# Performance work log

Hardware: AMD Instinct MI355X
Metric: run time of the kernel (lower is better)

## Reference

```python
import jax, jax.numpy as jnp
import numpy as np

N_NODES = 50000
N_EDGES = 1600000
IN_FEATS = 512
N_HIDDEN = 128
N_CLASSES = 40


def setup_inputs() -> dict:
    key = jax.random.key(0)
    k1, k2, k3, k4, k5, k6, k7 = jax.random.split(key, 7)
    features = jax.random.normal(k1, (N_NODES, IN_FEATS), dtype=jnp.float32)
    src = jax.random.randint(k2, (N_EDGES,), 0, N_NODES)
    dst = jax.random.randint(k3, (N_EDGES,), 0, N_NODES)
    # Glorot-ish init for weights, zeros for biases (DGL GraphConv defaults)
    W1 = jax.random.normal(k4, (IN_FEATS, N_HIDDEN), dtype=jnp.float32) / np.sqrt(IN_FEATS)
    b1 = jnp.zeros((N_HIDDEN,), dtype=jnp.float32)
    W2 = jax.random.normal(k5, (N_HIDDEN, N_CLASSES), dtype=jnp.float32) / np.sqrt(N_HIDDEN)
    b2 = jnp.zeros((N_CLASSES,), dtype=jnp.float32)
    return {"features": features, "W1": W1, "b1": b1, "W2": W2, "b2": b2,
            "src": src, "dst": dst}


def _norms(src, dst, n_nodes):
    ones = jnp.ones(src.shape[0], dtype=jnp.float32)
    deg_out = jax.ops.segment_sum(ones, src, num_segments=n_nodes)
    deg_in = jax.ops.segment_sum(ones, dst, num_segments=n_nodes)
    # clamp degree >= 1 as DGL does
    norm_src = jax.lax.rsqrt(jnp.maximum(deg_out, 1.0))
    norm_dst = jax.lax.rsqrt(jnp.maximum(deg_in, 1.0))
    return norm_src, norm_dst


def _graph_conv(x, W, b, src, dst, norm_src, norm_dst, n_nodes):
    # DGL GraphConv with norm='both'; in_feats > out_feats so W applied first
    h = x @ W                                   # [N, out]
    h = h * norm_src[:, None]                   # src-side D^{-1/2}
    msgs = h[src]                               # gather [E, out]
    agg = jax.ops.segment_sum(msgs, dst, num_segments=n_nodes)  # scatter-add
    agg = agg * norm_dst[:, None]               # dst-side D^{-1/2}
    return agg + b


def reference(features, W1, b1, W2, b2, src, dst):
    norm_src, norm_dst = _norms(src, dst, N_NODES)
    h = _graph_conv(features, W1, b1, src, dst, norm_src, norm_dst, N_NODES)
    h = jax.nn.relu(h)
    # dropout is identity at inference
    h = _graph_conv(h, W2, b2, src, dst, norm_src, norm_dst, N_NODES)
    return h
```

## Files before the change

### kernel.cpp

```cpp
#include <hip/hip_runtime.h>
#include <hip/hip_bf16.h>

#define N_NODES 50000
#define N_EDGES 1600000
#define IN_FEATS 512
#define N_HIDDEN 128
#define N_CLASSES 40
#define NBKT 782
#define NBLK 800
#define EPB 2000
#define NROWPAD 50048

typedef __attribute__((ext_vector_type(8))) short bf16x8;
typedef __attribute__((ext_vector_type(4))) float f32x4;

__device__ __forceinline__ unsigned short f2bf(float f) {
    unsigned u = __float_as_uint(f);
    u = (u + 0x7FFFu + ((u >> 16) & 1u)) >> 16;
    return (unsigned short)u;
}
__device__ __forceinline__ float bf2f(unsigned short h) {
    return __uint_as_float(((unsigned)h) << 16);
}
__device__ __forceinline__ unsigned pk_bf(float a, float b) {
    __hip_bfloat162 h = __float22bfloat162_rn(make_float2(a, b));
    union { __hip_bfloat162 v; unsigned u; } c;
    c.v = h;
    return c.u;
}

__global__ __launch_bounds__(256) void p1_hist(
    const int* __restrict__ src, const int* __restrict__ dst,
    int* __restrict__ histD, int* __restrict__ histS) {
    __shared__ int hd[NBKT], hs[NBKT];
    int t = threadIdx.x, b = blockIdx.x;
    for (int i = t; i < NBKT; i += 256) { hd[i] = 0; hs[i] = 0; }
    __syncthreads();
    int e0 = b * EPB;
    for (int i = t; i < EPB; i += 256) {
        atomicAdd(&hd[dst[e0 + i] >> 6], 1);
        atomicAdd(&hs[src[e0 + i] >> 6], 1);
    }
    __syncthreads();
    for (int i = t; i < NBKT; i += 256) {
        histD[b * NBKT + i] = hd[i];
        histS[b * NBKT + i] = hs[i];
    }
}

__global__ __launch_bounds__(256) void p2_local(
    const int* __restrict__ histD, const int* __restrict__ histS,
    int* __restrict__ baseD, int* __restrict__ baseS,
    int* __restrict__ totD, int* __restrict__ totS) {
    int wv = threadIdx.x >> 6, lane = threadIdx.x & 63;
    int w = blockIdx.x * 4 + wv;
    if (w >= NBKT) return;
    int runD = 0, runS = 0;
#pragma unroll
    for (int c = 0; c < 13; c++) {
        int blk = c * 64 + lane;
        int vD = 0, vS = 0;
        if (blk < NBLK) {
            vD = histD[blk * NBKT + w];
            vS = histS[blk * NBKT + w];
        }
        int iD = vD, iS = vS;
#pragma unroll
        for (int off = 1; off < 64; off <<= 1) {
            int tD = __shfl_up(iD, off);
            int tS = __shfl_up(iS, off);
            if (lane >= off) { iD += tD; iS += tS; }
        }
        if (blk < NBLK) {
            baseD[blk * NBKT + w] = runD + iD - vD;
            baseS[blk * NBKT + w] = runS + iS - vS;
        }
        runD += __shfl(iD, 63);
        runS += __shfl(iS, 63);
    }
    if (lane == 0) { totD[w] = runD; totS[w] = runS; }
}

__global__ __launch_bounds__(1024) void p2_small(
    const int* __restrict__ totD, const int* __restrict__ totS,
    int* __restrict__ bucket_base, int* __restrict__ srcb_base,
    int* __restrict__ offsets) {
    __shared__ int part[1024];
    int t = threadIdx.x;
    int v = (t < NBKT) ? totD[t] : 0;
    part[t] = v;
    __syncthreads();
    for (int off = 1; off < 1024; off <<= 1) {
        int x = (t >= off) ? part[t - off] : 0;
        __syncthreads();
        part[t] += x;
        __syncthreads();
    }
    if (t < NBKT) bucket_base[t] = part[t] - v;
    if (t == 0) { bucket_base[NBKT] = N_EDGES; offsets[N_NODES] = N_EDGES; }
    __syncthreads();
    v = (t < NBKT) ? totS[t] : 0;
    part[t] = v;
    __syncthreads();
    for (int off = 1; off < 1024; off <<= 1) {
        int x = (t >= off) ? part[t - off] : 0;
        __syncthreads();
        part[t] += x;
        __syncthreads();
    }
    if (t < NBKT) srcb_base[t] = part[t] - v;
    if (t == 0) srcb_base[NBKT] = N_EDGES;
}

__global__ __launch_bounds__(256) void p3_scatter(
    const int* __restrict__ src, const int* __restrict__ dst,
    const int* __restrict__ baseD, const int* __restrict__ baseS,
    const int* __restrict__ bucket_base, const int* __restrict__ srcb_base,
    unsigned int* __restrict__ edata, unsigned char* __restrict__ srcv) {
    __shared__ int curD[NBKT], curS[NBKT];
    int t = threadIdx.x, b = blockIdx.x;
    for (int i = t; i < NBKT; i += 256) {
        curD[i] = bucket_base[i] + baseD[b * NBKT + i];
        curS[i] = srcb_base[i] + baseS[b * NBKT + i];
    }
    __syncthreads();
    int e0 = b * EPB;
    for (int i = t; i < EPB; i += 256) {
        int s = src[e0 + i], d = dst[e0 + i];
        int slotD = atomicAdd(&curD[d >> 6], 1);
        edata[slotD] = (unsigned)s | ((unsigned)(d & 63) << 16);
        int slotS = atomicAdd(&curS[s >> 6], 1);
        srcv[slotS] = (unsigned char)(s & 63);
    }
}

__global__ __launch_bounds__(256) void p4_count(
    const int* __restrict__ srcb_base, const unsigned char* __restrict__ srcv,
    float* __restrict__ norm_src) {
    __shared__ int cnt[64];
    int t = threadIdx.x, b = blockIdx.x;
    if (t < 64) cnt[t] = 0;
    __syncthreads();
    int s0 = srcb_base[b], s1 = srcb_base[b + 1];
    for (int i = s0 + t; i < s1; i += 256) atomicAdd(&cnt[srcv[i]], 1);
    __syncthreads();
    if (t < 64) {
        int node = b * 64 + t;
        if (node < N_NODES) norm_src[node] = rsqrtf(fmaxf((float)cnt[t], 1.0f));
    }
}

__global__ __launch_bounds__(256) void p4_build(
    const int* __restrict__ bucket_base, const unsigned int* __restrict__ edata,
    int* __restrict__ offsets, float* __restrict__ norm_dst,
    int* __restrict__ sorted_src) {
    __shared__ int cnt[64], cur[64];
    int t = threadIdx.x, b = blockIdx.x;
    if (t < 64) cnt[t] = 0;
    __syncthreads();
    int s0 = bucket_base[b], s1 = bucket_base[b + 1];
    for (int i = s0 + t; i < s1; i += 256)
        atomicAdd(&cnt[(edata[i] >> 16) & 63], 1);
    __syncthreads();
    if (t == 0) {
        int run = 0;
        for (int i = 0; i < 64; i++) { cur[i] = run; run += cnt[i]; }
    }
    __syncthreads();
    if (t < 64) {
        int node = b * 64 + t;
        if (node < N_NODES) {
            offsets[node] = s0 + cur[t];
            norm_dst[node] = rsqrtf(fmaxf((float)cnt[t], 1.0f));
        }
    }
    __syncthreads();
    for (int i = s0 + t; i < s1; i += 256) {
        unsigned e = edata[i];
        int slot = atomicAdd(&cur[(e >> 16) & 63], 1);
        sorted_src[s0 + slot] = (int)(e & 0xFFFFu);
    }
}

__global__ __launch_bounds__(256) void w1cvt_kernel(const float* __restrict__ W1,
                                                    unsigned short* __restrict__ Wch,
                                                    unsigned short* __restrict__ Wcl) {
    int i = blockIdx.x * 256 + threadIdx.x;
    if (i >= IN_FEATS * N_HIDDEN) return;
    int k = i >> 7, c = i & 127;
    float v = W1[i];
    unsigned short h = f2bf(v);
    int o = (k >> 5) * 4096 + c * 32 + (k & 31);
    Wch[o] = h;
    Wcl[o] = f2bf(v - bf2f(h));
}

__global__ __launch_bounds__(256) void w2cvt_kernel(const float* __restrict__ W2,
                                                    unsigned short* __restrict__ Wth,
                                                    unsigned short* __restrict__ Wtl) {
    int i = blockIdx.x * 256 + threadIdx.x;
    if (i >= 48 * 128) return;
    int n = i >> 7, k = i & 127;
    float v = (n < N_CLASSES) ? W2[k * N_CLASSES + n] : 0.f;
    unsigned short h = f2bf(v);
    Wth[n * 128 + k] = h;
    Wtl[n * 128 + k] = f2bf(v - bf2f(h));
}

__global__ __launch_bounds__(256) void gemm1_kernel(
    const float* __restrict__ X, const unsigned short* __restrict__ Wch,
    const unsigned short* __restrict__ Wcl,
    const float* __restrict__ norm_src, unsigned short* __restrict__ Hb) {
    __shared__ __align__(16) unsigned short Xh[64][40];
    __shared__ __align__(16) unsigned short Xl[64][40];
    const int tid = threadIdx.x;
    const int lane = tid & 63;
    const int wv = tid >> 6;
    const int m = lane & 15;
    const int q = lane >> 4;
    const int row0 = blockIdx.x * 64;

    const int r0 = tid >> 3,          kq0 = (tid & 7) * 4;
    const int r1 = (tid + 256) >> 3,  kq1 = (tid & 7) * 4;
    const bool g0 = (row0 + r0) < N_NODES;
    const bool g1 = (row0 + r1) < N_NODES;
    const float* xp0 = &X[(size_t)(row0 + r0) * IN_FEATS + kq0];
    const float* xp1 = &X[(size_t)(row0 + r1) * IN_FEATS + kq1];

    f32x4 acc[4][2];
#pragma unroll
    for (int i = 0; i < 4; i++)
#pragma unroll
        for (int j = 0; j < 2; j++) acc[i][j] = (f32x4){0.f, 0.f, 0.f, 0.f};

    float4 xa0 = g0 ? *(const float4*)xp0 : make_float4(0.f, 0.f, 0.f, 0.f);
    float4 xa1 = g1 ? *(const float4*)xp1 : make_float4(0.f, 0.f, 0.f, 0.f);

    for (int kc = 0; kc < 16; kc++) {
        {
            unsigned h0 = pk_bf(xa0.x, xa0.y), h1 = pk_bf(xa0.z, xa0.w);
            unsigned l0 = pk_bf(xa0.x - __uint_as_float(h0 << 16),
                                xa0.y - __uint_as_float(h0 & 0xffff0000u));
            unsigned l1 = pk_bf(xa0.z - __uint_as_float(h1 << 16),
                                xa0.w - __uint_as_float(h1 & 0xffff0000u));
            *(uint2*)&Xh[r0][kq0] = make_uint2(h0, h1);
            *(uint2*)&Xl[r0][kq0] = make_uint2(l0, l1);
            unsigned h2 = pk_bf(xa1.x, xa1.y), h3 = pk_bf(xa1.z, xa1.w);
            unsigned l2 = pk_bf(xa1.x - __uint_as_float(h2 << 16),
                                xa1.y - __uint_as_float(h2 & 0xffff0000u));
            unsigned l3 = pk_bf(xa1.z - __uint_as_float(h3 << 16),
                                xa1.w - __uint_as_float(h3 & 0xffff0000u));
            *(uint2*)&Xh[r1][kq1] = make_uint2(h2, h3);
            *(uint2*)&Xl[r1][kq1] = make_uint2(l2, l3);
        }
        __syncthreads();
        if (kc < 15) {
            xa0 = g0 ? *(const float4*)(xp0 + (kc + 1) * 32) : make_float4(0.f, 0.f, 0.f, 0.f);
            xa1 = g1 ? *(const float4*)(xp1 + (kc + 1) * 32) : make_float4(0.f, 0.f, 0.f, 0.f);
        }
        bf16x8 bh[2], bl[2];
#pragma unroll
        for (int j = 0; j < 2; j++) {
            int o = kc * 4096 + (wv * 32 + j * 16 + m) * 32 + q * 8;
            bh[j] = *(const bf16x8*)&Wch[o];
            bl[j] = *(const bf16x8*)&Wcl[o];
        }
        bf16x8 ah[4], al[4];
#pragma unroll
        for (int i = 0; i < 4; i++) {
            ah[i] = *(const bf16x8*)&Xh[i * 16 + m][q * 8];
            al[i] = *(const bf16x8*)&Xl[i * 16 + m][q * 8];
        }
#pragma unroll
        for (int i = 0; i < 4; i++)
#pragma unroll
            for (int j = 0; j < 2; j++) {
                acc[i][j] = __builtin_amdgcn_mfma_f32_16x16x32_bf16(ah[i], bh[j], acc[i][j], 0, 0, 0);
                acc[i][j] = __builtin_amdgcn_mfma_f32_16x16x32_bf16(ah[i], bl[j], acc[i][j], 0, 0, 0);
                acc[i][j] = __builtin_amdgcn_mfma_f32_16x16x32_bf16(al[i], bh[j], acc[i][j], 0, 0, 0);
            }
        __syncthreads();
    }
#pragma unroll
    for (int i = 0; i < 4; i++) {
#pragma unroll
        for (int r = 0; r < 4; r++) {
            int grow = row0 + i * 16 + q * 4 + r;
            if (grow < N_NODES) {
                float sc = norm_src[grow];
#pragma unroll
                for (int j = 0; j < 2; j++)
                    Hb[(size_t)grow * N_HIDDEN + wv * 32 + j * 16 + m] = f2bf(acc[i][j][r] * sc);
            }
        }
    }
}

#define ADD8(W)                                               \
    acc0 += __uint_as_float((W).x << 16);                     \
    acc1 += __uint_as_float((W).x & 0xffff0000u);             \
    acc2 += __uint_as_float((W).y << 16);                     \
    acc3 += __uint_as_float((W).y & 0xffff0000u);             \
    acc4 += __uint_as_float((W).z << 16);                     \
    acc5 += __uint_as_float((W).z & 0xffff0000u);             \
    acc6 += __uint_as_float((W).w << 16);                     \
    acc7 += __uint_as_float((W).w & 0xffff0000u);

__global__ __launch_bounds__(256) void agg1_kernel(
    const int* __restrict__ offsets, const int* __restrict__ sorted_src,
    const unsigned short* __restrict__ Hb, const float* __restrict__ norm_dst,
    const float* __restrict__ norm_src, const float* __restrict__ b1,
    unsigned short* __restrict__ H1h, unsigned short* __restrict__ H1l) {
    int wid = (blockIdx.x * 256 + threadIdx.x) >> 6;
    int lane = threadIdx.x & 63;
    if (wid >= N_NODES) return;
    int start = offsets[wid], end = offsets[wid + 1];
    int quad = lane >> 4;
    int c8 = (lane & 15) * 8;
    float acc0 = 0.f, acc1 = 0.f, acc2 = 0.f, acc3 = 0.f;
    float acc4 = 0.f, acc5 = 0.f, acc6 = 0.f, acc7 = 0.f;
    int base = start;
    for (; base + 8 <= end; base += 8) {
        int e0 = sorted_src[base + quad];
        int e1 = sorted_src[base + 4 + quad];
        uint4 w0 = *(const uint4*)&Hb[(size_t)e0 * N_HIDDEN + c8];
        uint4 w1 = *(const uint4*)&Hb[(size_t)e1 * N_HIDDEN + c8];
        ADD8(w0);
        ADD8(w1);
    }
    int rem = end - base;
    if (quad < rem) {
        int e = sorted_src[base + quad];
        uint4 w = *(const uint4*)&Hb[(size_t)e * N_HIDDEN + c8];
        ADD8(w);
    }
    if (quad + 4 < rem) {
        int e = sorted_src[base + 4 + quad];
        uint4 w = *(const uint4*)&Hb[(size_t)e * N_HIDDEN + c8];
        ADD8(w);
    }
    acc0 += __shfl_xor(acc0, 16); acc0 += __shfl_xor(acc0, 32);
    acc1 += __shfl_xor(acc1, 16); acc1 += __shfl_xor(acc1, 32);
    acc2 += __shfl_xor(acc2, 16); acc2 += __shfl_xor(acc2, 32);
    acc3 += __shfl_xor(acc3, 16); acc3 += __shfl_xor(acc3, 32);
    acc4 += __shfl_xor(acc4, 16); acc4 += __shfl_xor(acc4, 32);
    acc5 += __shfl_xor(acc5, 16); acc5 += __shfl_xor(acc5, 32);
    acc6 += __shfl_xor(acc6, 16); acc6 += __shfl_xor(acc6, 32);
    acc7 += __shfl_xor(acc7, 16); acc7 += __shfl_xor(acc7, 32);
    if (quad == 0) {
        float nd = norm_dst[wid];
        float ns = norm_src[wid];
        float4 ba = *(const float4*)&b1[c8];
        float4 bb = *(const float4*)&b1[c8 + 4];
        float o[8];
        o[0] = fmaxf(acc0 * nd + ba.x, 0.f) * ns;
        o[1] = fmaxf(acc1 * nd + ba.y, 0.f) * ns;
        o[2] = fmaxf(acc2 * nd + ba.z, 0.f) * ns;
        o[3] = fmaxf(acc3 * nd + ba.w, 0.f) * ns;
        o[4] = fmaxf(acc4 * nd + bb.x, 0.f) * ns;
        o[5] = fmaxf(acc5 * nd + bb.y, 0.f) * ns;
        o[6] = fmaxf(acc6 * nd + bb.z, 0.f) * ns;
        o[7] = fmaxf(acc7 * nd + bb.w, 0.f) * ns;
        unsigned short hh[8], ll[8];
#pragma unroll
        for (int t = 0; t < 8; t++) {
            hh[t] = f2bf(o[t]);
            ll[t] = f2bf(o[t] - bf2f(hh[t]));
        }
        uint4 ph = make_uint4((unsigned)hh[0] | ((unsigned)hh[1] << 16),
                              (unsigned)hh[2] | ((unsigned)hh[3] << 16),
                              (unsigned)hh[4] | ((unsigned)hh[5] << 16),
                              (unsigned)hh[6] | ((unsigned)hh[7] << 16));
        uint4 pl = make_uint4((unsigned)ll[0] | ((unsigned)ll[1] << 16),
                              (unsigned)ll[2] | ((unsigned)ll[3] << 16),
                              (unsigned)ll[4] | ((unsigned)ll[5] << 16),
                              (unsigned)ll[6] | ((unsigned)ll[7] << 16));
        *(uint4*)&H1h[(size_t)wid * N_HIDDEN + c8] = ph;
        *(uint4*)&H1l[(size_t)wid * N_HIDDEN + c8] = pl;
    }
}

__global__ __launch_bounds__(256) void gemm2_kernel(
    const unsigned short* __restrict__ H1h, const unsigned short* __restrict__ H1l,
    const unsigned short* __restrict__ W2th, const unsigned short* __restrict__ W2tl,
    float* __restrict__ H2p) {
    __shared__ __align__(16) unsigned short Bh[48][136];
    __shared__ __align__(16) unsigned short Bl[48][136];
    const int tid = threadIdx.x;
    for (int i = tid; i < 48 * 16; i += 256) {
        int n = i >> 4, kq = (i & 15) * 8;
        *(uint4*)&Bh[n][kq] = *(const uint4*)&W2th[n * 128 + kq];
        *(uint4*)&Bl[n][kq] = *(const uint4*)&W2tl[n * 128 + kq];
    }
    __syncthreads();
    const int lane = tid & 63;
    const int wave = tid >> 6;
    const int m = lane & 15;
    const int q = lane >> 4;
    const int row0 = blockIdx.x * 128 + wave * 32;

    f32x4 acc[2][3];
#pragma unroll
    for (int i = 0; i < 2; i++)
#pragma unroll
        for (int j = 0; j < 3; j++) acc[i][j] = (f32x4){0.f, 0.f, 0.f, 0.f};

#pragma unroll
    for (int kc = 0; kc < 4; kc++) {
        bf16x8 bh[3], bl[3];
#pragma unroll
        for (int j = 0; j < 3; j++) {
            bh[j] = *(const bf16x8*)&Bh[j * 16 + m][kc * 32 + q * 8];
            bl[j] = *(const bf16x8*)&Bl[j * 16 + m][kc * 32 + q * 8];
        }
#pragma unroll
        for (int i = 0; i < 2; i++) {
            size_t ro = (size_t)(row0 + i * 16 + m) * N_HIDDEN + kc * 32 + q * 8;
            bf16x8 ah = *(const bf16x8*)&H1h[ro];
            bf16x8 al = *(const bf16x8*)&H1l[ro];
#pragma unroll
            for (int j = 0; j < 3; j++) {
                acc[i][j] = __builtin_amdgcn_mfma_f32_16x16x32_bf16(ah, bh[j], acc[i][j], 0, 0, 0);
                acc[i][j] = __builtin_amdgcn_mfma_f32_16x16x32_bf16(ah, bl[j], acc[i][j], 0, 0, 0);
                acc[i][j] = __builtin_amdgcn_mfma_f32_16x16x32_bf16(al, bh[j], acc[i][j], 0, 0, 0);
            }
        }
    }
#pragma unroll
    for (int i = 0; i < 2; i++) {
#pragma unroll
        for (int r = 0; r < 4; r++) {
            int row = row0 + i * 16 + q * 4 + r;
            if (row < N_NODES) {
#pragma unroll
                for (int j = 0; j < 3; j++) {
                    int col = j * 16 + m;
                    if (col < N_CLASSES)
                        H2p[(size_t)row * 64 + col] = acc[i][j][r];
                }
            }
        }
    }
}

__global__ __launch_bounds__(256) void agg2_kernel(
    const int* __restrict__ offsets, const int* __restrict__ sorted_src,
    const float* __restrict__ H2p, const float* __restrict__ norm_dst,
    const float* __restrict__ b2, float* __restrict__ OUT) {
    int wid = (blockIdx.x * 256 + threadIdx.x) >> 6;
    int lane = threadIdx.x & 63;
    if (wid >= N_NODES) return;
    int start = offsets[wid], end = offsets[wid + 1];
    int quad = lane >> 4;
    int c4 = (lane & 15) * 4;
    bool active = c4 < N_CLASSES;
    float4 acc = make_float4(0.f, 0.f, 0.f, 0.f);
    int base = start;
    int nfull = (end - start) & ~7;
    for (; base < start + nfull; base += 8) {
        int e0 = sorted_src[base + quad];
        int e1 = sorted_src[base + 4 + quad];
        if (active) {
            float4 v0 = *(const float4*)&H2p[(size_t)e0 * 64 + c4];
            float4 v1 = *(const float4*)&H2p[(size_t)e1 * 64 + c4];
            acc.x += v0.x + v1.x;
            acc.y += v0.y + v1.y;
            acc.z += v0.z + v1.z;
            acc.w += v0.w + v1.w;
        }
    }
    int rem = end - base;
    int n4 = rem & ~3;
    for (int t = 0; t < n4; t += 4) {
        int e = sorted_src[base + t + quad];
        if (active) {
            float4 v = *(const float4*)&H2p[(size_t)e * 64 + c4];
            acc.x += v.x; acc.y += v.y; acc.z += v.z; acc.w += v.w;
        }
    }
    base += n4;
    if (quad < end - base && active) {
        int e = sorted_src[base + quad];
        float4 v = *(const float4*)&H2p[(size_t)e * 64 + c4];
        acc.x += v.x; acc.y += v.y; acc.z += v.z; acc.w += v.w;
    }
    acc.x += __shfl_xor(acc.x, 16); acc.x += __shfl_xor(acc.x, 32);
    acc.y += __shfl_xor(acc.y, 16); acc.y += __shfl_xor(acc.y, 32);
    acc.z += __shfl_xor(acc.z, 16); acc.z += __shfl_xor(acc.z, 32);
    acc.w += __shfl_xor(acc.w, 16); acc.w += __shfl_xor(acc.w, 32);
    if (lane < 10) {
        float nd = norm_dst[wid];
        float4 b = *(const float4*)&b2[lane * 4];
        acc.x = acc.x * nd + b.x;
        acc.y = acc.y * nd + b.y;
        acc.z = acc.z * nd + b.z;
        acc.w = acc.w * nd + b.w;
        *(float4*)&OUT[(size_t)wid * N_CLASSES + lane * 4] = acc;
    }
}

extern "C" void kernel_launch(void* const* d_in, const int* in_sizes, int n_in,
                              void* d_out, int out_size, void* d_ws, size_t ws_size,
                              hipStream_t stream) {
    const float* X   = (const float*)d_in[0];
    const float* W1  = (const float*)d_in[1];
    const float* b1  = (const float*)d_in[2];
    const float* W2  = (const float*)d_in[3];
    const float* b2  = (const float*)d_in[4];
    const int*   src = (const int*)d_in[5];
    const int*   dst = (const int*)d_in[6];
    float* out = (float*)d_out;

    float* norm_src   = (float*)d_ws;
    float* norm_dst   = norm_src + N_NODES;
    int*   offsets    = (int*)(norm_dst + N_NODES);
    int*   bucket_base = offsets + N_NODES + 16;
    int*   srcb_base  = bucket_base + 800;
    unsigned int* edata = (unsigned int*)(srcb_base + 800);
    unsigned char* srcv = (unsigned char*)(edata + N_EDGES);
    int*   sorted_src = (int*)(edata + N_EDGES) + 400000;
    int*   regionA    = sorted_src + N_EDGES;
    int*   histD      = regionA;
    int*   histS      = regionA + 625600;
    int*   baseD      = regionA + 1251200;
    int*   baseS      = regionA + 1876800;
    int*   totD       = regionA + 2502400;
    int*   totS       = regionA + 2503200;
    unsigned short* Hb = (unsigned short*)regionA;
    float* H2p        = (float*)regionA;
    unsigned short* H1h = (unsigned short*)(regionA + 3200000);
    unsigned short* H1l = H1h + (size_t)NROWPAD * N_HIDDEN;
    unsigned short* W1ch = H1l + (size_t)NROWPAD * N_HIDDEN;
    unsigned short* W1cl = W1ch + IN_FEATS * N_HIDDEN;
    unsigned short* W2th = W1cl + IN_FEATS * N_HIDDEN;
    unsigned short* W2tl = W2th + 48 * 128;

    p1_hist<<<NBLK, 256, 0, stream>>>(src, dst, histD, histS);
    p2_local<<<(NBKT + 3) / 4, 256, 0, stream>>>(histD, histS, baseD, baseS, totD, totS);
    p2_small<<<1, 1024, 0, stream>>>(totD, totS, bucket_base, srcb_base, offsets);
    p3_scatter<<<NBLK, 256, 0, stream>>>(src, dst, baseD, baseS, bucket_base, srcb_base,
                                         edata, srcv);
    p4_count<<<NBKT, 256, 0, stream>>>(srcb_base, srcv, norm_src);
    p4_build<<<NBKT, 256, 0, stream>>>(bucket_base, edata, offsets, norm_dst, sorted_src);

    w1cvt_kernel<<<(IN_FEATS * N_HIDDEN + 255) / 256, 256, 0, stream>>>(W1, W1ch, W1cl);
    w2cvt_kernel<<<(48 * 128 + 255) / 256, 256, 0, stream>>>(W2, W2th, W2tl);
    gemm1_kernel<<<NBKT, 256, 0, stream>>>(X, W1ch, W1cl, norm_src, Hb);
    agg1_kernel<<<(N_NODES + 3) / 4, 256, 0, stream>>>(offsets, sorted_src, Hb, norm_dst,
                                                       norm_src, b1, H1h, H1l);
    gemm2_kernel<<<(N_NODES + 127) / 128, 256, 0, stream>>>(H1h, H1l, W2th, W2tl, H2p);
    agg2_kernel<<<(N_NODES + 3) / 4, 256, 0, stream>>>(offsets, sorted_src, H2p, norm_dst, b2, out);
}
```

Baseline: 383.9 us.

## Fuse histogram with GEMM1, merge weight conversions and degree kernels, apply src norm in aggregation

The edge histogram pass and the first GEMM now run as one launch whose blocks are split by index, so the GEMM no longer waits for the graph preprocessing chain. For that, the source-side normalization moves out of GEMM1 into agg1, which loads norm_src per edge and uses FMA. The two weight conversion kernels and the two degree/build kernels are each merged into one launch, and both aggregation loops are unrolled to 16 edges. The cost is an extra random norm_src load per gathered edge in agg1, and Hb moves to its own buffer so it is not overwritten by the histogram data.

```diff
diff --git a/kernel.cpp b/kernel.cpp
--- a/kernel.cpp
+++ b/kernel.cpp
@@ -29,196 +29,59 @@
     return c.u;
 }
 
-__global__ __launch_bounds__(256) void p1_hist(
+__global__ __launch_bounds__(256) void setup_cvt(
+    const float* __restrict__ W1, const float* __restrict__ W2,
+    unsigned short* __restrict__ W1ch, unsigned short* __restrict__ W1cl,
+    unsigned short* __restrict__ W2th, unsigned short* __restrict__ W2tl) {
+    int i = blockIdx.x * 256 + threadIdx.x;
+    if (i < IN_FEATS * N_HIDDEN) {
+        int k = i >> 7, c = i & 127;
+        float v = W1[i];
+        unsigned short h = f2bf(v);
+        int o = (k >> 5) * 4096 + c * 32 + (k & 31);
+        W1ch[o] = h;
+        W1cl[o] = f2bf(v - bf2f(h));
+    } else {
+        int j = i - IN_FEATS * N_HIDDEN;
+        int n = j >> 7, k = j & 127;
+        float v = (n < N_CLASSES) ? W2[k * N_CLASSES + n] : 0.f;
+        unsigned short h = f2bf(v);
+        W2th[n * 128 + k] = h;
+        W2tl[n * 128 + k] = f2bf(v - bf2f(h));
+    }
+}
+
+__global__ __launch_bounds__(256) void megaA(
     const int* __restrict__ src, const int* __restrict__ dst,
-    int* __restrict__ histD, int* __restrict__ histS) {
+    int* __restrict__ histD, int* __restrict__ histS,
+    const float* __restrict__ X, const unsigned short* __restrict__ Wch,
+    const unsigned short* __restrict__ Wcl, unsigned short* __restrict__ Hb) {
     __shared__ int hd[NBKT], hs[NBKT];
-    int t = threadIdx.x, b = blockIdx.x;
-    for (int i = t; i < NBKT; i += 256) { hd[i] = 0; hs[i] = 0; }
-    __syncthreads();
-    int e0 = b * EPB;
-    for (int i = t; i < EPB; i += 256) {
-        atomicAdd(&hd[dst[e0 + i] >> 6], 1);
-        atomicAdd(&hs[src[e0 + i] >> 6], 1);
-    }
-    __syncthreads();
-    for (int i = t; i < NBKT; i += 256) {
-        histD[b * NBKT + i] = hd[i];
-        histS[b * NBKT + i] = hs[i];
-    }
-}
-
-__global__ __launch_bounds__(256) void p2_local(
-    const int* __restrict__ histD, const int* __restrict__ histS,
-    int* __restrict__ baseD, int* __restrict__ baseS,
-    int* __restrict__ totD, int* __restrict__ totS) {
-    int wv = threadIdx.x >> 6, lane = threadIdx.x & 63;
-    int w = blockIdx.x * 4 + wv;
-    if (w >= NBKT) return;
-    int runD = 0, runS = 0;
-#pragma unroll
-    for (int c = 0; c < 13; c++) {
-        int blk = c * 64 + lane;
-        int vD = 0, vS = 0;
-        if (blk < NBLK) {
-            vD = histD[blk * NBKT + w];
-            vS = histS[blk * NBKT + w];
-        }
-        int iD = vD, iS = vS;
-#pragma unroll
-        for (int off = 1; off < 64; off <<= 1) {
-            int tD = __shfl_up(iD, off);
-            int tS = __shfl_up(iS, off);
-            if (lane >= off) { iD += tD; iS += tS; }
-        }
-        if (blk < NBLK) {
-            baseD[blk * NBKT + w] = runD + iD - vD;
-            baseS[blk * NBKT + w] = runS + iS - vS;
-        }
-        runD += __shfl(iD, 63);
-        runS += __shfl(iS, 63);
-    }
-    if (lane == 0) { totD[w] = runD; totS[w] = runS; }
-}
-
-__global__ __launch_bounds__(1024) void p2_small(
-    const int* __restrict__ totD, const int* __restrict__ totS,
-    int* __restrict__ bucket_base, int* __restrict__ srcb_base,
-    int* __restrict__ offsets) {
-    __shared__ int part[1024];
-    int t = threadIdx.x;
-    int v = (t < NBKT) ? totD[t] : 0;
-    part[t] = v;
-    __syncthreads();
-    for (int off = 1; off < 1024; off <<= 1) {
-        int x = (t >= off) ? part[t - off] : 0;
-        __syncthreads();
-        part[t] += x;
-        __syncthreads();
-    }
-    if (t < NBKT) bucket_base[t] = part[t] - v;
-    if (t == 0) { bucket_base[NBKT] = N_EDGES; offsets[N_NODES] = N_EDGES; }
-    __syncthreads();
-    v = (t < NBKT) ? totS[t] : 0;
-    part[t] = v;
-    __syncthreads();
-    for (int off = 1; off < 1024; off <<= 1) {
-        int x = (t >= off) ? part[t - off] : 0;
-        __syncthreads();
-        part[t] += x;
-        __syncthreads();
-    }
-    if (t < NBKT) srcb_base[t] = part[t] - v;
-    if (t == 0) srcb_base[NBKT] = N_EDGES;
-}
-
-__global__ __launch_bounds__(256) void p3_scatter(
-    const int* __restrict__ src, const int* __restrict__ dst,
-    const int* __restrict__ baseD, const int* __restrict__ baseS,
-    const int* __restrict__ bucket_base, const int* __restrict__ srcb_base,
-    unsigned int* __restrict__ edata, unsigned char* __restrict__ srcv) {
-    __shared__ int curD[NBKT], curS[NBKT];
-    int t = threadIdx.x, b = blockIdx.x;
-    for (int i = t; i < NBKT; i += 256) {
-        curD[i] = bucket_base[i] + baseD[b * NBKT + i];
-        curS[i] = srcb_base[i] + baseS[b * NBKT + i];
-    }
-    __syncthreads();
-    int e0 = b * EPB;
-    for (int i = t; i < EPB; i += 256) {
-        int s = src[e0 + i], d = dst[e0 + i];
-        int slotD = atomicAdd(&curD[d >> 6], 1);
-        edata[slotD] = (unsigned)s | ((unsigned)(d & 63) << 16);
-        int slotS = atomicAdd(&curS[s >> 6], 1);
-        srcv[slotS] = (unsigned char)(s & 63);
-    }
-}
-
-__global__ __launch_bounds__(256) void p4_count(
-    const int* __restrict__ srcb_base, const unsigned char* __restrict__ srcv,
-    float* __restrict__ norm_src) {
-    __shared__ int cnt[64];
-    int t = threadIdx.x, b = blockIdx.x;
-    if (t < 64) cnt[t] = 0;
-    __syncthreads();
-    int s0 = srcb_base[b], s1 = srcb_base[b + 1];
-    for (int i = s0 + t; i < s1; i += 256) atomicAdd(&cnt[srcv[i]], 1);
-    __syncthreads();
-    if (t < 64) {
-        int node = b * 64 + t;
-        if (node < N_NODES) norm_src[node] = rsqrtf(fmaxf((float)cnt[t], 1.0f));
-    }
-}
-
-__global__ __launch_bounds__(256) void p4_build(
-    const int* __restrict__ bucket_base, const unsigned int* __restrict__ edata,
-    int* __restrict__ offsets, float* __restrict__ norm_dst,
-    int* __restrict__ sorted_src) {
-    __shared__ int cnt[64], cur[64];
-    int t = threadIdx.x, b = blockIdx.x;
-    if (t < 64) cnt[t] = 0;
-    __syncthreads();
-    int s0 = bucket_base[b], s1 = bucket_base[b + 1];
-    for (int i = s0 + t; i < s1; i += 256)
-        atomicAdd(&cnt[(edata[i] >> 16) & 63], 1);
-    __syncthreads();
-    if (t == 0) {
-        int run = 0;
-        for (int i = 0; i < 64; i++) { cur[i] = run; run += cnt[i]; }
-    }
-    __syncthreads();
-    if (t < 64) {
-        int node = b * 64 + t;
-        if (node < N_NODES) {
-            offsets[node] = s0 + cur[t];
-            norm_dst[node] = rsqrtf(fmaxf((float)cnt[t], 1.0f));
-        }
-    }
-    __syncthreads();
-    for (int i = s0 + t; i < s1; i += 256) {
-        unsigned e = edata[i];
-        int slot = atomicAdd(&cur[(e >> 16) & 63], 1);
-        sorted_src[s0 + slot] = (int)(e & 0xFFFFu);
-    }
-}
-
-__global__ __launch_bounds__(256) void w1cvt_kernel(const float* __restrict__ W1,
-                                                    unsigned short* __restrict__ Wch,
-                                                    unsigned short* __restrict__ Wcl) {
-    int i = blockIdx.x * 256 + threadIdx.x;
-    if (i >= IN_FEATS * N_HIDDEN) return;
-    int k = i >> 7, c = i & 127;
-    float v = W1[i];
-    unsigned short h = f2bf(v);
-    int o = (k >> 5) * 4096 + c * 32 + (k & 31);
-    Wch[o] = h;
-    Wcl[o] = f2bf(v - bf2f(h));
-}
-
-__global__ __launch_bounds__(256) void w2cvt_kernel(const float* __restrict__ W2,
-                                                    unsigned short* __restrict__ Wth,
-                                                    unsigned short* __restrict__ Wtl) {
-    int i = blockIdx.x * 256 + threadIdx.x;
-    if (i >= 48 * 128) return;
-    int n = i >> 7, k = i & 127;
-    float v = (n < N_CLASSES) ? W2[k * N_CLASSES + n] : 0.f;
-    unsigned short h = f2bf(v);
-    Wth[n * 128 + k] = h;
-    Wtl[n * 128 + k] = f2bf(v - bf2f(h));
-}
-
-__global__ __launch_bounds__(256) void gemm1_kernel(
-    const float* __restrict__ X, const unsigned short* __restrict__ Wch,
-    const unsigned short* __restrict__ Wcl,
-    const float* __restrict__ norm_src, unsigned short* __restrict__ Hb) {
     __shared__ __align__(16) unsigned short Xh[64][40];
     __shared__ __align__(16) unsigned short Xl[64][40];
     const int tid = threadIdx.x;
+
+    if (blockIdx.x < NBLK) {
+        int b = blockIdx.x;
+        for (int i = tid; i < NBKT; i += 256) { hd[i] = 0; hs[i] = 0; }
+        __syncthreads();
+        int e0 = b * EPB;
+        for (int i = tid; i < EPB; i += 256) {
+            atomicAdd(&hd[dst[e0 + i] >> 6], 1);
+            atomicAdd(&hs[src[e0 + i] >> 6], 1);
+        }
+        __syncthreads();
+        for (int i = tid; i < NBKT; i += 256) {
+            histD[b * NBKT + i] = hd[i];
+            histS[b * NBKT + i] = hs[i];
+        }
+        return;
+    }
     const int lane = tid & 63;
     const int wv = tid >> 6;
     const int m = lane & 15;
     const int q = lane >> 4;
-    const int row0 = blockIdx.x * 64;
+    const int row0 = (blockIdx.x - NBLK) * 64;
 
     const int r0 = tid >> 3,          kq0 = (tid & 7) * 4;
     const int r1 = (tid + 256) >> 3,  kq1 = (tid & 7) * 4;
@@ -287,24 +150,145 @@
         for (int r = 0; r < 4; r++) {
             int grow = row0 + i * 16 + q * 4 + r;
             if (grow < N_NODES) {
-                float sc = norm_src[grow];
 #pragma unroll
                 for (int j = 0; j < 2; j++)
-                    Hb[(size_t)grow * N_HIDDEN + wv * 32 + j * 16 + m] = f2bf(acc[i][j][r] * sc);
+                    Hb[(size_t)grow * N_HIDDEN + wv * 32 + j * 16 + m] = f2bf(acc[i][j][r]);
             }
         }
     }
 }
 
-#define ADD8(W)                                               \
-    acc0 += __uint_as_float((W).x << 16);                     \
-    acc1 += __uint_as_float((W).x & 0xffff0000u);             \
-    acc2 += __uint_as_float((W).y << 16);                     \
-    acc3 += __uint_as_float((W).y & 0xffff0000u);             \
-    acc4 += __uint_as_float((W).z << 16);                     \
-    acc5 += __uint_as_float((W).z & 0xffff0000u);             \
-    acc6 += __uint_as_float((W).w << 16);                     \
-    acc7 += __uint_as_float((W).w & 0xffff0000u);
+__global__ __launch_bounds__(256) void p2_local(
+    const int* __restrict__ histD, const int* __restrict__ histS,
+    int* __restrict__ baseD, int* __restrict__ baseS,
+    int* __restrict__ totD, int* __restrict__ totS) {
+    int wv = threadIdx.x >> 6, lane = threadIdx.x & 63;
+    int w = blockIdx.x * 4 + wv;
+    if (w >= NBKT) return;
+    int runD = 0, runS = 0;
+#pragma unroll
+    for (int c = 0; c < 13; c++) {
+        int blk = c * 64 + lane;
+        int vD = 0, vS = 0;
+        if (blk < NBLK) {
+            vD = histD[blk * NBKT + w];
+            vS = histS[blk * NBKT + w];
+        }
+        int iD = vD, iS = vS;
+#pragma unroll
+        for (int off = 1; off < 64; off <<= 1) {
+            int tD = __shfl_up(iD, off);
+            int tS = __shfl_up(iS, off);
+            if (lane >= off) { iD += tD; iS += tS; }
+        }
+        if (blk < NBLK) {
+            baseD[blk * NBKT + w] = runD + iD - vD;
+            baseS[blk * NBKT + w] = runS + iS - vS;
+        }
+        runD += __shfl(iD, 63);
+        runS += __shfl(iS, 63);
+    }
+    if (lane == 0) { totD[w] = runD; totS[w] = runS; }
+}
+
+__global__ __launch_bounds__(1024) void p2_small(
+    const int* __restrict__ totD, const int* __restrict__ totS,
+    int* __restrict__ bucket_base, int* __restrict__ srcb_base,
+    int* __restrict__ offsets) {
+    __shared__ int part[1024];
+    int t = threadIdx.x;
+    int v = (t < NBKT) ? totD[t] : 0;
+    part[t] = v;
+    __syncthreads();
+    for (int off = 1; off < 1024; off <<= 1) {
+        int x = (t >= off) ? part[t - off] : 0;
+        __syncthreads();
+        part[t] += x;
+        __syncthreads();
+    }
+    if (t < NBKT) bucket_base[t] = part[t] - v;
+    if (t == 0) { bucket_base[NBKT] = N_EDGES; offsets[N_NODES] = N_EDGES; }
+    __syncthreads();
+    v = (t < NBKT) ? totS[t] : 0;
+    part[t] = v;
+    __syncthreads();
+    for (int off = 1; off < 1024; off <<= 1) {
+        int x = (t >= off) ? part[t - off] : 0;
+        __syncthreads();
+        part[t] += x;
+        __syncthreads();
+    }
+    if (t < NBKT) srcb_base[t] = part[t] - v;
+    if (t == 0) srcb_base[NBKT] = N_EDGES;
+}
+
+__global__ __launch_bounds__(256) void p3_scatter(
+    const int* __restrict__ src, const int* __restrict__ dst,
+    const int* __restrict__ baseD, const int* __restrict__ baseS,
+    const int* __restrict__ bucket_base, const int* __restrict__ srcb_base,
+    unsigned int* __restrict__ edata, unsigned char* __restrict__ srcv) {
+    __shared__ int curD[NBKT], curS[NBKT];
+    int t = threadIdx.x, b = blockIdx.x;
+    for (int i = t; i < NBKT; i += 256) {
+        curD[i] = bucket_base[i] + baseD[b * NBKT + i];
+        curS[i] = srcb_base[i] + baseS[b * NBKT + i];
+    }
+    __syncthreads();
+    int e0 = b * EPB;
+    for (int i = t; i < EPB; i += 256) {
+        int s = src[e0 + i], d = dst[e0 + i];
+        int slotD = atomicAdd(&curD[d >> 6], 1);
+        edata[slotD] = (unsigned)s | ((unsigned)(d & 63) << 16);
+        int slotS = atomicAdd(&curS[s >> 6], 1);
+        srcv[slotS] = (unsigned char)(s & 63);
+    }
+}
+
+__global__ __launch_bounds__(256) void p4_fused(
+    const int* __restrict__ srcb_base, const unsigned char* __restrict__ srcv,
+    const int* __restrict__ bucket_base, const unsigned int* __restrict__ edata,
+    int* __restrict__ offsets, float* __restrict__ norm_src,
+    float* __restrict__ norm_dst, int* __restrict__ sorted_src) {
+    __shared__ int cntS[64], cntD[64], cur[64];
+    int t = threadIdx.x, b = blockIdx.x;
+    if (t < 64) { cntS[t] = 0; cntD[t] = 0; }
+    __syncthreads();
+    int s0 = srcb_base[b], s1 = srcb_base[b + 1];
+    for (int i = s0 + t; i < s1; i += 256) atomicAdd(&cntS[srcv[i]], 1);
+    int d0 = bucket_base[b], d1 = bucket_base[b + 1];
+    for (int i = d0 + t; i < d1; i += 256)
+        atomicAdd(&cntD[(edata[i] >> 16) & 63], 1);
+    __syncthreads();
+    if (t == 0) {
+        int run = 0;
+        for (int i = 0; i < 64; i++) { cur[i] = run; run += cntD[i]; }
+    }
+    __syncthreads();
+    if (t < 64) {
+        int node = b * 64 + t;
+        if (node < N_NODES) {
+            norm_src[node] = rsqrtf(fmaxf((float)cntS[t], 1.0f));
+            offsets[node] = d0 + cur[t];
+            norm_dst[node] = rsqrtf(fmaxf((float)cntD[t], 1.0f));
+        }
+    }
+    __syncthreads();
+    for (int i = d0 + t; i < d1; i += 256) {
+        unsigned e = edata[i];
+        int slot = atomicAdd(&cur[(e >> 16) & 63], 1);
+        sorted_src[d0 + slot] = (int)(e & 0xFFFFu);
+    }
+}
+
+#define FMA8(W, NS)                                                   \
+    acc0 = fmaf(__uint_as_float((W).x << 16), NS, acc0);              \
+    acc1 = fmaf(__uint_as_float((W).x & 0xffff0000u), NS, acc1);      \
+    acc2 = fmaf(__uint_as_float((W).y << 16), NS, acc2);              \
+    acc3 = fmaf(__uint_as_float((W).y & 0xffff0000u), NS, acc3);      \
+    acc4 = fmaf(__uint_as_float((W).z << 16), NS, acc4);              \
+    acc5 = fmaf(__uint_as_float((W).z & 0xffff0000u), NS, acc5);      \
+    acc6 = fmaf(__uint_as_float((W).w << 16), NS, acc6);              \
+    acc7 = fmaf(__uint_as_float((W).w & 0xffff0000u), NS, acc7);
 
 __global__ __launch_bounds__(256) void agg1_kernel(
     const int* __restrict__ offsets, const int* __restrict__ sorted_src,
@@ -320,24 +304,34 @@
     float acc0 = 0.f, acc1 = 0.f, acc2 = 0.f, acc3 = 0.f;
     float acc4 = 0.f, acc5 = 0.f, acc6 = 0.f, acc7 = 0.f;
     int base = start;
-    for (; base + 8 <= end; base += 8) {
+    for (; base + 16 <= end; base += 16) {
         int e0 = sorted_src[base + quad];
         int e1 = sorted_src[base + 4 + quad];
+        int e2 = sorted_src[base + 8 + quad];
+        int e3 = sorted_src[base + 12 + quad];
+        float n0 = norm_src[e0], n1 = norm_src[e1];
+        float n2 = norm_src[e2], n3 = norm_src[e3];
         uint4 w0 = *(const uint4*)&Hb[(size_t)e0 * N_HIDDEN + c8];
         uint4 w1 = *(const uint4*)&Hb[(size_t)e1 * N_HIDDEN + c8];
-        ADD8(w0);
-        ADD8(w1);
+        uint4 w2 = *(const uint4*)&Hb[(size_t)e2 * N_HIDDEN + c8];
+        uint4 w3 = *(const uint4*)&Hb[(size_t)e3 * N_HIDDEN + c8];
+        FMA8(w0, n0);
+        FMA8(w1, n1);
+        FMA8(w2, n2);
+        FMA8(w3, n3);
+    }
+    for (; base + 4 <= end; base += 4) {
+        int e = sorted_src[base + quad];
+        float n = norm_src[e];
+        uint4 w = *(const uint4*)&Hb[(size_t)e * N_HIDDEN + c8];
+        FMA8(w, n);
     }
     int rem = end - base;
     if (quad < rem) {
         int e = sorted_src[base + quad];
+        float n = norm_src[e];
         uint4 w = *(const uint4*)&Hb[(size_t)e * N_HIDDEN + c8];
-        ADD8(w);
-    }
-    if (quad + 4 < rem) {
-        int e = sorted_src[base + 4 + quad];
-        uint4 w = *(const uint4*)&Hb[(size_t)e * N_HIDDEN + c8];
-        ADD8(w);
+        FMA8(w, n);
     }
     acc0 += __shfl_xor(acc0, 16); acc0 += __shfl_xor(acc0, 32);
     acc1 += __shfl_xor(acc1, 16); acc1 += __shfl_xor(acc1, 32);
@@ -456,30 +450,31 @@
     bool active = c4 < N_CLASSES;
     float4 acc = make_float4(0.f, 0.f, 0.f, 0.f);
     int base = start;
-    int nfull = (end - start) & ~7;
-    for (; base < start + nfull; base += 8) {
+    for (; base + 16 <= end; base += 16) {
         int e0 = sorted_src[base + quad];
         int e1 = sorted_src[base + 4 + quad];
+        int e2 = sorted_src[base + 8 + quad];
+        int e3 = sorted_src[base + 12 + quad];
         if (active) {
             float4 v0 = *(const float4*)&H2p[(size_t)e0 * 64 + c4];
             float4 v1 = *(const float4*)&H2p[(size_t)e1 * 64 + c4];
-            acc.x += v0.x + v1.x;
-            acc.y += v0.y + v1.y;
-            acc.z += v0.z + v1.z;
-            acc.w += v0.w + v1.w;
-        }
-    }
-    int rem = end - base;
-    int n4 = rem & ~3;
-    for (int t = 0; t < n4; t += 4) {
-        int e = sorted_src[base + t + quad];
+            float4 v2 = *(const float4*)&H2p[(size_t)e2 * 64 + c4];
+            float4 v3 = *(const float4*)&H2p[(size_t)e3 * 64 + c4];
+            acc.x += (v0.x + v1.x) + (v2.x + v3.x);
+            acc.y += (v0.y + v1.y) + (v2.y + v3.y);
+            acc.z += (v0.z + v1.z) + (v2.z + v3.z);
+            acc.w += (v0.w + v1.w) + (v2.w + v3.w);
+        }
+    }
+    for (; base + 4 <= end; base += 4) {
+        int e = sorted_src[base + quad];
         if (active) {
             float4 v = *(const float4*)&H2p[(size_t)e * 64 + c4];
             acc.x += v.x; acc.y += v.y; acc.z += v.z; acc.w += v.w;
         }
     }
-    base += n4;
-    if (quad < end - base && active) {
+    int rem = end - base;
+    if (quad < rem && active) {
         int e = sorted_src[base + quad];
         float4 v = *(const float4*)&H2p[(size_t)e * 64 + c4];
         acc.x += v.x; acc.y += v.y; acc.z += v.z; acc.w += v.w;
@@ -526,7 +521,6 @@
     int*   baseS      = regionA + 1876800;
     int*   totD       = regionA + 2502400;
     int*   totS       = regionA + 2503200;
-    unsigned short* Hb = (unsigned short*)regionA;
     float* H2p        = (float*)regionA;
     unsigned short* H1h = (unsigned short*)(regionA + 3200000);
     unsigned short* H1l = H1h + (size_t)NROWPAD * N_HIDDEN;
@@ -534,18 +528,17 @@
     unsigned short* W1cl = W1ch + IN_FEATS * N_HIDDEN;
     unsigned short* W2th = W1cl + IN_FEATS * N_HIDDEN;
     unsigned short* W2tl = W2th + 48 * 128;
-
-    p1_hist<<<NBLK, 256, 0, stream>>>(src, dst, histD, histS);
+    unsigned short* Hb   = W2tl + 48 * 128;
+
+    setup_cvt<<<(IN_FEATS * N_HIDDEN + 48 * 128) / 256, 256, 0, stream>>>(
+        W1, W2, W1ch, W1cl, W2th, W2tl);
+    megaA<<<NBLK + NBKT, 256, 0, stream>>>(src, dst, histD, histS, X, W1ch, W1cl, Hb);
     p2_local<<<(NBKT + 3) / 4, 256, 0, stream>>>(histD, histS, baseD, baseS, totD, totS);
     p2_small<<<1, 1024, 0, stream>>>(totD, totS, bucket_base, srcb_base, offsets);
     p3_scatter<<<NBLK, 256, 0, stream>>>(src, dst, baseD, baseS, bucket_base, srcb_base,
                                          edata, srcv);
-    p4_count<<<NBKT, 256, 0, stream>>>(srcb_base, srcv, norm_src);
-    p4_build<<<NBKT, 256, 0, stream>>>(bucket_base, edata, offsets, norm_dst, sorted_src);
-
-    w1cvt_kernel<<<(IN_FEATS * N_HIDDEN + 255) / 256, 256, 0, stream>>>(W1, W1ch, W1cl);
-    w2cvt_kernel<<<(48 * 128 + 255) / 256, 256, 0, stream>>>(W2, W2th, W2tl);
-    gemm1_kernel<<<NBKT, 256, 0, stream>>>(X, W1ch, W1cl, norm_src, Hb);
+    p4_fused<<<NBKT, 256, 0, stream>>>(srcb_base, srcv, bucket_base, edata,
+                                       offsets, norm_src, norm_dst, sorted_src);
     agg1_kernel<<<(N_NODES + 3) / 4, 256, 0, stream>>>(offsets, sorted_src, Hb, norm_dst,
                                                        norm_src, b1, H1h, H1l);
     gemm2_kernel<<<(N_NODES + 127) / 128, 256, 0, stream>>>(H1h, H1l, W2th, W2tl, H2p);
```

After: 371.5 us. 3.2% less time.
